# Performance work log

Hardware: AMD Instinct MI355X
Metric: run time of the kernel (lower is better)

The kernel has to match this reference:

```python
import jax, jax.numpy as jnp
import numpy as np

N = 50000        # nodes
E = 800000       # edges (before self loops)
NFEAT = 128
HEADS = 8
NHID = 16
SLOPE = 0.2      # PyG GATConv default negative_slope


def gat_conv(x, src, dst, W, a_src, a_dst, bias, heads, out_ch, concat):
    n = x.shape[0]
    h = (x @ W).reshape(n, heads, out_ch)                 # [N,H,C]
    al_s = jnp.sum(h * a_src, axis=-1)                    # [N,H]
    al_d = jnp.sum(h * a_dst, axis=-1)                    # [N,H]
    # add self loops (PyG GATConv default add_self_loops=True)
    loop = jnp.arange(n, dtype=src.dtype)
    s = jnp.concatenate([src, loop])
    d = jnp.concatenate([dst, loop])
    e = jax.nn.leaky_relu(al_s[s] + al_d[d], SLOPE)       # [E+N,H]
    # numerically stable softmax over incoming edges of each dst node
    emax = jax.lax.stop_gradient(jax.ops.segment_max(e, d, num_segments=n))
    ex = jnp.exp(e - emax[d])
    denom = jax.ops.segment_sum(ex, d, num_segments=n)
    alpha = ex / denom[d]                                 # [E+N,H]
    out = jax.ops.segment_sum(h[s] * alpha[:, :, None], d, num_segments=n)  # [N,H,C]
    out = out.reshape(n, heads * out_ch) if concat else out.mean(axis=1)
    return out + bias


def setup_inputs() -> dict:
    key = jax.random.key(0)
    ks = jax.random.split(key, 11)
    x = jax.random.normal(ks[0], (N, NFEAT), jnp.float32)
    src = jax.random.randint(ks[1], (E,), 0, N, dtype=jnp.int32)
    dst = jax.random.randint(ks[2], (E,), 0, N, dtype=jnp.int32)
    dst = jnp.where(src == dst, (dst + 1) % N, dst)  # no pre-existing self loops
    edge_index = jnp.stack([src, dst])
    sc = 0.1
    W1 = jax.random.normal(ks[3], (NFEAT, HEADS * NHID), jnp.float32) * sc
    a_src1 = jax.random.normal(ks[4], (HEADS, NHID), jnp.float32) * sc
    a_dst1 = jax.random.normal(ks[5], (HEADS, NHID), jnp.float32) * sc
    b1 = jnp.zeros((HEADS * NHID,), jnp.float32)
    W2 = jax.random.normal(ks[6], (HEADS * NHID, NHID), jnp.float32) * sc
    a_src2 = jax.random.normal(ks[7], (1, NHID), jnp.float32) * sc
    a_dst2 = jax.random.normal(ks[8], (1, NHID), jnp.float32) * sc
    b2 = jnp.zeros((NHID,), jnp.float32)
    return {"x": x, "edge_index": edge_index, "W1": W1, "a_src1": a_src1,
            "a_dst1": a_dst1, "b1": b1, "W2": W2, "a_src2": a_src2,
            "a_dst2": a_dst2, "b2": b2}


def reference(x, edge_index, W1, a_src1, a_dst1, b1, W2, a_src2, a_dst2, b2):
    src, dst = edge_index[0], edge_index[1]
    # layer 1: GATConv(nfeat -> nhid, heads=8, concat) + relu (dropout off in eval)
    h = jax.nn.relu(gat_conv(x, src, dst, W1, a_src1, a_dst1, b1, HEADS, NHID, True))
    # layer 2: GATConv(heads*nhid -> nhid, heads=1, concat=False) + relu
    out = jax.nn.relu(gat_conv(h, src, dst, W2, a_src2, a_dst2, b2, 1, NHID, False))
    return out
```

## Files before the change

kernel.cpp:

```cpp
#include <hip/hip_runtime.h>

#define NFEAT 128
#define HEADS 8
#define NHID 16
#define SLOPE 0.2f
#define BSH 8
#define CAPSH 13

typedef __fp16 f16x8 __attribute__((ext_vector_type(8)));
typedef __fp16 f16x2 __attribute__((ext_vector_type(2)));
typedef float  f4v   __attribute__((ext_vector_type(4)));

__device__ __forceinline__ unsigned pack2h(float a, float b) {
    union { f16x2 h; unsigned u; } r;
    r.h = __builtin_amdgcn_cvt_pkrtz(a, b);
    return r.u;
}
__device__ __forceinline__ f16x2 as_f16x2(unsigned u) {
    union { unsigned u; f16x2 h; } r; r.u = u; return r.h;
}
__device__ __forceinline__ f16x8 frag_from_f32(const float* p) {
    float4 q0 = *(const float4*)p;
    float4 q1 = *(const float4*)(p + 4);
    union { f16x8 v; f16x2 h[4]; } r;
    r.h[0] = __builtin_amdgcn_cvt_pkrtz(q0.x, q0.y);
    r.h[1] = __builtin_amdgcn_cvt_pkrtz(q0.z, q0.w);
    r.h[2] = __builtin_amdgcn_cvt_pkrtz(q1.x, q1.y);
    r.h[3] = __builtin_amdgcn_cvt_pkrtz(q1.z, q1.w);
    return r.v;
}


__global__ __launch_bounds__(256) void k_bscatter(const int* __restrict__ src,
                                                  const int* __restrict__ dst,
                                                  int E, int chunk,
                                                  int* __restrict__ bcount,
                                                  unsigned* __restrict__ pairs) {
    __shared__ int cnt[256], base[256];
    int t = threadIdx.x;
    int beg = blockIdx.x * chunk;
    int end = min(beg + chunk, E);
    if (beg >= end) return;
    cnt[t] = 0;
    __syncthreads();
    for (int i = beg + t; i < end; i += 256)
        atomicAdd(&cnt[dst[i] >> BSH], 1);
    __syncthreads();
    int c = cnt[t];
    base[t] = c ? (atomicAdd(&bcount[t], c) + (t << CAPSH)) : 0;
    __syncthreads();
    cnt[t] = 0;
    __syncthreads();
    for (int i = beg + t; i < end; i += 256) {
        int d = dst[i];
        int b = d >> BSH;
        int ofs = atomicAdd(&cnt[b], 1);
        pairs[base[b] + ofs] = (unsigned)src[i] | ((unsigned)(d & 255) << 16);
    }
}


__global__ __launch_bounds__(256) void k_scan_prep(const int* __restrict__ bcount,
                                                   int* __restrict__ cstart,
                                                   int* __restrict__ row_start,
                                                   int E, int n,
                                                   const float* __restrict__ W1,
                                                   const float* __restrict__ as1,
                                                   const float* __restrict__ ad1,
                                                   const float* __restrict__ W2,
                                                   unsigned* __restrict__ Wt1,
                                                   __fp16* __restrict__ Aat1,
                                                   unsigned* __restrict__ W2t) {
    if (blockIdx.x == 0) {
        __shared__ int sh[256];
        int t = threadIdx.x;
        int nb = (n + 255) >> BSH;
        int v = (t < nb) ? bcount[t] : 0;
        sh[t] = v;
        __syncthreads();
        for (int off = 1; off < 256; off <<= 1) {
            int u = (t >= off) ? sh[t - off] : 0;
            __syncthreads();
            sh[t] += u;
            __syncthreads();
        }
        cstart[t] = sh[t] - v;
        if (t == 0) row_start[n] = E + n;
        return;
    }
    int t = (blockIdx.x - 1) * 256 + threadIdx.x;
    if (t < 8192) {
        int c = t >> 6, m = t & 63;
        int k = 2 * m;
        Wt1[t] = pack2h(W1[k * 128 + c], W1[(k + 1) * 128 + c]);
    } else if (t < 10240) {
        int idx = t - 8192;
        int j = idx >> 7, k = idx & 127;
        float v = 0.f;
        if (j < 8)  { if ((k >> 4) == j)     v = as1[k]; }
        else        { if ((k >> 4) == j - 8) v = ad1[k]; }
        Aat1[idx] = (__fp16)v;
    } else if (t < 11264) {
        int idx = t - 10240;
        int c = idx >> 6, m = idx & 63;
        int k = 2 * m;
        W2t[idx] = pack2h(W2[k * 16 + c], W2[(k + 1) * 16 + c]);
    }
}


__global__ __launch_bounds__(256) void k_csr_gemm1(const unsigned* __restrict__ pairs,
                                                   const int* __restrict__ bcount,
                                                   const int* __restrict__ cstart,
                                                   int* __restrict__ row_start,
                                                   unsigned short* __restrict__ csr,
                                                   const float* __restrict__ xf,
                                                   const __fp16* __restrict__ Wt,
                                                   const __fp16* __restrict__ Aat,
                                                   unsigned* __restrict__ h1u,
                                                   float* __restrict__ als,
                                                   float* __restrict__ ald,
                                                   int n, int nbuck) {
    __shared__ unsigned smem[4][32 * 64];
    if ((int)blockIdx.x < nbuck) {
        int* deg = (int*)&smem[0][0];
        int* sc  = deg + 256;
        int b = blockIdx.x, t = threadIdx.x;
        int d0 = b << BSH;
        int nd = min(256, n - d0);
        deg[t] = (t < nd) ? 1 : 0;
        __syncthreads();
        int pbeg = b << CAPSH, pend = pbeg + bcount[b];
        for (int i = pbeg + t; i < pend; i += 256)
            atomicAdd(&deg[(pairs[i] >> 16) & 255], 1);
        __syncthreads();
        int v = deg[t];
        sc[t] = v;
        __syncthreads();
        for (int off = 1; off < 256; off <<= 1) {
            int u = (t >= off) ? sc[t - off] : 0;
            __syncthreads();
            sc[t] += u;
            __syncthreads();
        }
        int excl = sc[t] - v;
        int cbase = cstart[b] + d0;
        if (t < nd) row_start[d0 + t] = cbase + excl;
        __syncthreads();
        deg[t] = excl;
        __syncthreads();
        if (t < nd) {
            int pos = atomicAdd(&deg[t], 1);
            csr[cbase + pos] = (unsigned short)(d0 + t);
        }
        for (int i = pbeg + t; i < pend; i += 256) {
            unsigned p = pairs[i];
            int pos = atomicAdd(&deg[(p >> 16) & 255], 1);
            csr[cbase + pos] = (unsigned short)(p & 0xFFFFu);
        }
        return;
    }
    int bid = blockIdx.x - nbuck;
    int tid = threadIdx.x;
    int w = tid >> 6, l = tid & 63;
    int l15 = l & 15, lq = l >> 4;
    int wbase = bid * 128 + w * 32;
    f4v acc[2][8] = {};
    int r0 = min(wbase + l15, n - 1);
    int r1 = min(wbase + 16 + l15, n - 1);
#pragma unroll
    for (int kb = 0; kb < 4; ++kb) {
        int ko = kb * 32 + lq * 8;
        f16x8 a0 = frag_from_f32(&xf[(size_t)r0 * 128 + ko]);
        f16x8 a1 = frag_from_f32(&xf[(size_t)r1 * 128 + ko]);
#pragma unroll
        for (int cg = 0; cg < 8; ++cg) {
            f16x8 b = *(const f16x8*)&Wt[(size_t)(cg * 16 + l15) * 128 + ko];
            acc[0][cg] = __builtin_amdgcn_mfma_f32_16x16x32_f16(a0, b, acc[0][cg], 0, 0, 0);
            acc[1][cg] = __builtin_amdgcn_mfma_f32_16x16x32_f16(a1, b, acc[1][cg], 0, 0, 0);
        }
    }
    unsigned* myl = smem[w];
#pragma unroll
    for (int T = 0; T < 2; ++T) {
#pragma unroll
        for (int cg = 0; cg < 8; ++cg) {
#pragma unroll
            for (int j = 0; j < 4; ++j) {
                float v = acc[T][cg][j];
                float vo = __shfl_xor(v, 1);
                if ((l15 & 1) == 0) {
                    int nd = T * 16 + lq * 4 + j;
                    int wd = cg * 8 + (l15 >> 1);
                    int widx = nd * 64 + (((wd >> 2) ^ (nd & 15)) << 2) + (wd & 3);
                    myl[widx] = pack2h(v, vo);
                }
            }
        }
    }
    __syncthreads();
#pragma unroll
    for (int it = 0; it < 8; ++it) {
        int nd = it * 4 + lq;
        int node = wbase + nd;
        uint4 vv = *(const uint4*)&myl[nd * 64 + ((l15 ^ (nd & 15)) << 2)];
        if (node < n) *(uint4*)&h1u[(size_t)node * 64 + l15 * 4] = vv;
    }
#pragma unroll
    for (int T = 0; T < 2; ++T) {
        f4v acca = {};
#pragma unroll
        for (int kb = 0; kb < 4; ++kb) {
            int nd = T * 16 + l15;
            f16x8 ah = *(const f16x8*)&myl[nd * 64 + (((kb * 4 + lq) ^ (nd & 15)) << 2)];
            f16x8 bb = *(const f16x8*)&Aat[l15 * 128 + kb * 32 + lq * 8];
            acca = __builtin_amdgcn_mfma_f32_16x16x32_f16(ah, bb, acca, 0, 0, 0);
        }
#pragma unroll
        for (int j = 0; j < 4; ++j) {
            int node = wbase + T * 16 + lq * 4 + j;
            if (node < n) {
                if (l15 < 8) als[(size_t)node * 8 + l15] = acca[j];
                else         ald[(size_t)node * 8 + (l15 - 8)] = acca[j];
            }
        }
    }
}


__global__ __launch_bounds__(256) void k_agg1(const unsigned* __restrict__ hu,
                                              const float* __restrict__ als,
                                              const float* __restrict__ ald,
                                              const float* __restrict__ bias,
                                              const int* __restrict__ row_start,
                                              const unsigned short* __restrict__ csr,
                                              unsigned* __restrict__ out1u, int n) {
    int t = threadIdx.x;
    int l = t & 63;
    int lc = l & 15, eg = l >> 4;
    int nn = blockIdx.x * 4 + (t >> 6);
    if (nn >= n) return;
    int beg = row_start[nn], end = row_start[nn + 1];
    int len = end - beg;
    int g0 = beg + ((len * eg) >> 2);
    int g1 = beg + ((len * (eg + 1)) >> 2);
    int hd = lc >> 1;
    float aldv = ald[(size_t)nn * 8 + hd];
    float a[8] = {0.f, 0.f, 0.f, 0.f, 0.f, 0.f, 0.f, 0.f};
    float dn = 0.f;
    f16x2 one2; one2[0] = (__fp16)1.f; one2[1] = (__fp16)1.f;
    int i = g0;
    for (; i + 4 <= g1; i += 4) {
        int s0 = csr[i], s1 = csr[i + 1], s2 = csr[i + 2], s3 = csr[i + 3];
        float e0 = als[(size_t)s0 * 8 + hd];
        float e1 = als[(size_t)s1 * 8 + hd];
        float e2 = als[(size_t)s2 * 8 + hd];
        float e3 = als[(size_t)s3 * 8 + hd];
        uint4 v0 = *(const uint4*)&hu[(size_t)s0 * 64 + lc * 4];
        uint4 v1 = *(const uint4*)&hu[(size_t)s1 * 64 + lc * 4];
        uint4 v2 = *(const uint4*)&hu[(size_t)s2 * 64 + lc * 4];
        uint4 v3 = *(const uint4*)&hu[(size_t)s3 * 64 + lc * 4];
        e0 += aldv; e0 = (e0 < 0.f) ? SLOPE * e0 : e0;
        e1 += aldv; e1 = (e1 < 0.f) ? SLOPE * e1 : e1;
        e2 += aldv; e2 = (e2 < 0.f) ? SLOPE * e2 : e2;
        e3 += aldv; e3 = (e3 < 0.f) ? SLOPE * e3 : e3;
        f16x2 xa = __builtin_amdgcn_cvt_pkrtz(__expf(e0), __expf(e1));
        f16x2 xb = __builtin_amdgcn_cvt_pkrtz(__expf(e2), __expf(e3));
        dn = __builtin_amdgcn_fdot2(xa, one2, dn, false);
        dn = __builtin_amdgcn_fdot2(xb, one2, dn, false);
        unsigned V0[4] = {v0.x, v0.y, v0.z, v0.w};
        unsigned V1[4] = {v1.x, v1.y, v1.z, v1.w};
        unsigned V2[4] = {v2.x, v2.y, v2.z, v2.w};
        unsigned V3[4] = {v3.x, v3.y, v3.z, v3.w};
#pragma unroll
        for (int j = 0; j < 4; ++j) {
            unsigned lo01 = __builtin_amdgcn_perm(V1[j], V0[j], 0x05040100u);
            unsigned hi01 = __builtin_amdgcn_perm(V1[j], V0[j], 0x07060302u);
            unsigned lo23 = __builtin_amdgcn_perm(V3[j], V2[j], 0x05040100u);
            unsigned hi23 = __builtin_amdgcn_perm(V3[j], V2[j], 0x07060302u);
            a[2 * j]     = __builtin_amdgcn_fdot2(xa, as_f16x2(lo01), a[2 * j], false);
            a[2 * j + 1] = __builtin_amdgcn_fdot2(xa, as_f16x2(hi01), a[2 * j + 1], false);
            a[2 * j]     = __builtin_amdgcn_fdot2(xb, as_f16x2(lo23), a[2 * j], false);
            a[2 * j + 1] = __builtin_amdgcn_fdot2(xb, as_f16x2(hi23), a[2 * j + 1], false);
        }
    }
    for (; i + 2 <= g1; i += 2) {
        int s0 = csr[i];
        int s1 = csr[i + 1];
        float e0 = als[(size_t)s0 * 8 + hd];
        float e1 = als[(size_t)s1 * 8 + hd];
        uint4 v0 = *(const uint4*)&hu[(size_t)s0 * 64 + lc * 4];
        uint4 v1 = *(const uint4*)&hu[(size_t)s1 * 64 + lc * 4];
        e0 += aldv; e0 = (e0 < 0.f) ? SLOPE * e0 : e0;
        e1 += aldv; e1 = (e1 < 0.f) ? SLOPE * e1 : e1;
        f16x2 xx = __builtin_amdgcn_cvt_pkrtz(__expf(e0), __expf(e1));
        dn = __builtin_amdgcn_fdot2(xx, one2, dn, false);
        unsigned V0[4] = {v0.x, v0.y, v0.z, v0.w};
        unsigned V1[4] = {v1.x, v1.y, v1.z, v1.w};
#pragma unroll
        for (int j = 0; j < 4; ++j) {
            unsigned lo = __builtin_amdgcn_perm(V1[j], V0[j], 0x05040100u);
            unsigned hi = __builtin_amdgcn_perm(V1[j], V0[j], 0x07060302u);
            a[2 * j]     = __builtin_amdgcn_fdot2(xx, as_f16x2(lo), a[2 * j], false);
            a[2 * j + 1] = __builtin_amdgcn_fdot2(xx, as_f16x2(hi), a[2 * j + 1], false);
        }
    }
    if (i < g1) {
        int s0 = csr[i];
        float e0 = als[(size_t)s0 * 8 + hd] + aldv;
        uint4 v0 = *(const uint4*)&hu[(size_t)s0 * 64 + lc * 4];
        e0 = (e0 < 0.f) ? SLOPE * e0 : e0;
        float x0 = __expf(e0);
        dn += x0;
        unsigned V0[4] = {v0.x, v0.y, v0.z, v0.w};
#pragma unroll
        for (int j = 0; j < 4; ++j) {
            f16x2 p = as_f16x2(V0[j]);
            a[2 * j]     = fmaf(x0, (float)p[0], a[2 * j]);
            a[2 * j + 1] = fmaf(x0, (float)p[1], a[2 * j + 1]);
        }
    }
#pragma unroll
    for (int j = 0; j < 8; ++j) {
        a[j] += __shfl_xor(a[j], 16);
        a[j] += __shfl_xor(a[j], 32);
    }
    dn += __shfl_xor(dn, 16);
    dn += __shfl_xor(dn, 32);
    if (eg == 0) {
        float inv = 1.f / dn;
        float4 b0 = *(const float4*)&bias[lc * 8];
        float4 b1 = *(const float4*)&bias[lc * 8 + 4];
        uint4 o;
        o.x = pack2h(fmaxf(a[0] * inv + b0.x, 0.f), fmaxf(a[1] * inv + b0.y, 0.f));
        o.y = pack2h(fmaxf(a[2] * inv + b0.z, 0.f), fmaxf(a[3] * inv + b0.w, 0.f));
        o.z = pack2h(fmaxf(a[4] * inv + b1.x, 0.f), fmaxf(a[5] * inv + b1.y, 0.f));
        o.w = pack2h(fmaxf(a[6] * inv + b1.z, 0.f), fmaxf(a[7] * inv + b1.w, 0.f));
        *(uint4*)&out1u[(size_t)nn * 64 + lc * 4] = o;
    }
}


__global__ __launch_bounds__(256) void k_gemm2m(const __fp16* __restrict__ o1,
                                                const __fp16* __restrict__ W2t,
                                                const float* __restrict__ as2,
                                                const float* __restrict__ ad2,
                                                __fp16* __restrict__ h2,
                                                float* __restrict__ als,
                                                float* __restrict__ ald, int n) {
    int tid = threadIdx.x;
    int w = tid >> 6, l = tid & 63;
    int l15 = l & 15, lq = l >> 4;
    int wbase = blockIdx.x * 128 + w * 32;
    f4v acc[2] = {};
    int r0 = min(wbase + l15, n - 1);
    int r1 = min(wbase + 16 + l15, n - 1);
#pragma unroll
    for (int kb = 0; kb < 4; ++kb) {
        int ko = kb * 32 + lq * 8;
        f16x8 a0 = *(const f16x8*)&o1[(size_t)r0 * 128 + ko];
        f16x8 a1 = *(const f16x8*)&o1[(size_t)r1 * 128 + ko];
        f16x8 b  = *(const f16x8*)&W2t[(size_t)l15 * 128 + ko];
        acc[0] = __builtin_amdgcn_mfma_f32_16x16x32_f16(a0, b, acc[0], 0, 0, 0);
        acc[1] = __builtin_amdgcn_mfma_f32_16x16x32_f16(a1, b, acc[1], 0, 0, 0);
    }
    float asv = as2[l15], adv = ad2[l15];
#pragma unroll
    for (int T = 0; T < 2; ++T) {
#pragma unroll
        for (int j = 0; j < 4; ++j) {
            int node = wbase + T * 16 + lq * 4 + j;
            float hv = acc[T][j];
            float ps = hv * asv, pd = hv * adv;
            ps += __shfl_xor(ps, 1); ps += __shfl_xor(ps, 2);
            ps += __shfl_xor(ps, 4); ps += __shfl_xor(ps, 8);
            pd += __shfl_xor(pd, 1); pd += __shfl_xor(pd, 2);
            pd += __shfl_xor(pd, 4); pd += __shfl_xor(pd, 8);
            if (node < n) {
                h2[(size_t)node * 16 + l15] = (__fp16)hv;
                if (l15 == 0) { als[node] = ps; ald[node] = pd; }
            }
        }
    }
}


__global__ __launch_bounds__(256) void k_agg2(const __fp16* __restrict__ h,
                                              const float* __restrict__ als,
                                              const float* __restrict__ ald,
                                              const float* __restrict__ bias,
                                              const int* __restrict__ row_start,
                                              const unsigned short* __restrict__ csr,
                                              float* __restrict__ out, int n) {
    int t = threadIdx.x;
    int l = t & 63;
    int lc = l & 15, eg = l >> 4;
    int nn = blockIdx.x * 4 + (t >> 6);
    if (nn >= n) return;
    int beg = row_start[nn], end = row_start[nn + 1];
    int len = end - beg;
    int g0 = beg + ((len * eg) >> 2);
    int g1 = beg + ((len * (eg + 1)) >> 2);
    float aldv = ald[nn];
    float ac0 = 0.f, ac1 = 0.f, ac2 = 0.f, ac3 = 0.f;
    float dn0 = 0.f, dn1 = 0.f, dn2 = 0.f, dn3 = 0.f;
    int i = g0;
    for (; i + 4 <= g1; i += 4) {
        int s0 = csr[i], s1 = csr[i + 1], s2 = csr[i + 2], s3 = csr[i + 3];
        float e0 = als[s0], e1 = als[s1], e2 = als[s2], e3 = als[s3];
        float v0 = (float)h[(size_t)s0 * 16 + lc];
        float v1 = (float)h[(size_t)s1 * 16 + lc];
        float v2 = (float)h[(size_t)s2 * 16 + lc];
        float v3 = (float)h[(size_t)s3 * 16 + lc];
        e0 += aldv; e0 = (e0 < 0.f) ? SLOPE * e0 : e0;
        e1 += aldv; e1 = (e1 < 0.f) ? SLOPE * e1 : e1;
        e2 += aldv; e2 = (e2 < 0.f) ? SLOPE * e2 : e2;
        e3 += aldv; e3 = (e3 < 0.f) ? SLOPE * e3 : e3;
        float x0 = __expf(e0), x1 = __expf(e1), x2 = __expf(e2), x3 = __expf(e3);
        dn0 += x0; dn1 += x1; dn2 += x2; dn3 += x3;
        ac0 = fmaf(x0, v0, ac0);
        ac1 = fmaf(x1, v1, ac1);
        ac2 = fmaf(x2, v2, ac2);
        ac3 = fmaf(x3, v3, ac3);
    }
    for (; i < g1; ++i) {
        int s0 = csr[i];
        float e0 = als[s0] + aldv;
        e0 = (e0 < 0.f) ? SLOPE * e0 : e0;
        float x0 = __expf(e0);
        dn0 += x0;
        ac0 = fmaf(x0, (float)h[(size_t)s0 * 16 + lc], ac0);
    }
    float ac = (ac0 + ac1) + (ac2 + ac3);
    float dn = (dn0 + dn1) + (dn2 + dn3);
    ac += __shfl_xor(ac, 16); ac += __shfl_xor(ac, 32);
    dn += __shfl_xor(dn, 16); dn += __shfl_xor(dn, 32);
    if (eg == 0) out[(size_t)nn * 16 + lc] = fmaxf(ac / dn + bias[lc], 0.f);
}


extern "C" void kernel_launch(void* const* d_in, const int* in_sizes, int n_in,
                              void* d_out, int out_size, void* d_ws, size_t ws_size,
                              hipStream_t stream) {
    const float* x   = (const float*)d_in[0];
    const int*   ei  = (const int*)d_in[1];
    const float* W1  = (const float*)d_in[2];
    const float* as1 = (const float*)d_in[3];
    const float* ad1 = (const float*)d_in[4];
    const float* b1  = (const float*)d_in[5];
    const float* W2  = (const float*)d_in[6];
    const float* as2 = (const float*)d_in[7];
    const float* ad2 = (const float*)d_in[8];
    const float* b2  = (const float*)d_in[9];

    int N = in_sizes[0] / NFEAT;
    int E = in_sizes[1] / 2;
    const int* srcp = ei;
    const int* dstp = ei + E;
    int NBUCK = (N + 255) >> BSH;
    int NBg = (N + 127) / 128;

    char* ws = (char*)d_ws;
    size_t off = 0;
    auto take = [&](size_t bytes) -> char* {
        char* p = ws + off;
        off = (off + bytes + 255) & ~(size_t)255;
        return p;
    };
    int*            row_start = (int*)take((size_t)(N + 1) * 4);
    int*            bcount    = (int*)take(256 * 4);
    int*            cstart    = (int*)take(256 * 4);
    unsigned*       pairs     = (unsigned*)take((size_t)256 << (CAPSH + 2));
    unsigned short* csr       = (unsigned short*)take((size_t)(E + N) * 2);
    unsigned*       Wt1       = (unsigned*)take((size_t)128 * 64 * 4);
    __fp16*         Aat1      = (__fp16*)take((size_t)16 * 128 * 2);
    unsigned*       W2t       = (unsigned*)take((size_t)16 * 64 * 4);
    unsigned*       h1u       = (unsigned*)take((size_t)N * 64 * 4);
    float*          als1      = (float*)take((size_t)N * 8 * 4);
    float*          ald1      = (float*)take((size_t)N * 8 * 4);
    unsigned*       out1u     = (unsigned*)take((size_t)N * 64 * 4);
    __fp16*         h2        = (__fp16*)take((size_t)N * 16 * 2);
    float*          als2      = (float*)take((size_t)N * 4);
    float*          ald2      = (float*)take((size_t)N * 4);

    hipMemsetAsync(bcount, 0, 256 * 4, stream);
    int chunk = (E + 127) / 128;
    k_bscatter<<<128, 256, 0, stream>>>(srcp, dstp, E, chunk, bcount, pairs);
    k_scan_prep<<<45, 256, 0, stream>>>(bcount, cstart, row_start, E, N,
                                        W1, as1, ad1, W2, Wt1, Aat1, W2t);
    k_csr_gemm1<<<NBUCK + NBg, 256, 0, stream>>>(pairs, bcount, cstart, row_start, csr,
                                                 x, (const __fp16*)Wt1, Aat1,
                                                 h1u, als1, ald1, N, NBUCK);
    k_agg1<<<(N + 3) / 4, 256, 0, stream>>>(h1u, als1, ald1, b1, row_start, csr, out1u, N);
    k_gemm2m<<<NBg, 256, 0, stream>>>((const __fp16*)out1u, (const __fp16*)W2t,
                                      as2, ad2, h2, als2, ald2, N);
    k_agg2<<<(N + 3) / 4, 256, 0, stream>>>(h2, als2, ald2, b2, row_start, csr, (float*)d_out, N);
}
```

Baseline: 121.9 us.

## Fuse layer-2 projection into layer-1 aggregation and widen edge scatter grid

The layer-2 linear projection and attention-logit computation move into the epilogue of the layer-1 aggregation kernel. Each wave stages its aggregated fp16 row in shared memory and computes the 16 outputs with packed fp16 dot products. This removes the out1 intermediate round-trip through global memory and one kernel launch, at the cost of a longer epilogue and extra shuffles in the aggregation kernel. Separately, the edge bucket-scatter kernel is launched with twice as many blocks over smaller chunks.

```diff
diff --git a/kernel.cpp b/kernel.cpp
--- a/kernel.cpp
+++ b/kernel.cpp
@@ -234,11 +234,18 @@
                                               const float* __restrict__ bias,
                                               const int* __restrict__ row_start,
                                               const unsigned short* __restrict__ csr,
-                                              unsigned* __restrict__ out1u, int n) {
+                                              const unsigned* __restrict__ W2t,
+                                              const float* __restrict__ as2,
+                                              const float* __restrict__ ad2,
+                                              __fp16* __restrict__ h2,
+                                              float* __restrict__ als2,
+                                              float* __restrict__ ald2, int n) {
+    __shared__ unsigned lrow[4][64];
     int t = threadIdx.x;
+    int w = t >> 6;
     int l = t & 63;
     int lc = l & 15, eg = l >> 4;
-    int nn = blockIdx.x * 4 + (t >> 6);
+    int nn = blockIdx.x * 4 + w;
     if (nn >= n) return;
     int beg = row_start[nn], end = row_start[nn + 1];
     int len = end - beg;
@@ -327,8 +334,8 @@
     }
     dn += __shfl_xor(dn, 16);
     dn += __shfl_xor(dn, 32);
+    float inv = 1.f / dn;
     if (eg == 0) {
-        float inv = 1.f / dn;
         float4 b0 = *(const float4*)&bias[lc * 8];
         float4 b1 = *(const float4*)&bias[lc * 8 + 4];
         uint4 o;
@@ -336,52 +343,30 @@
         o.y = pack2h(fmaxf(a[2] * inv + b0.z, 0.f), fmaxf(a[3] * inv + b0.w, 0.f));
         o.z = pack2h(fmaxf(a[4] * inv + b1.x, 0.f), fmaxf(a[5] * inv + b1.y, 0.f));
         o.w = pack2h(fmaxf(a[6] * inv + b1.z, 0.f), fmaxf(a[7] * inv + b1.w, 0.f));
-        *(uint4*)&out1u[(size_t)nn * 64 + lc * 4] = o;
-    }
-}
-
-
-__global__ __launch_bounds__(256) void k_gemm2m(const __fp16* __restrict__ o1,
-                                                const __fp16* __restrict__ W2t,
-                                                const float* __restrict__ as2,
-                                                const float* __restrict__ ad2,
-                                                __fp16* __restrict__ h2,
-                                                float* __restrict__ als,
-                                                float* __restrict__ ald, int n) {
-    int tid = threadIdx.x;
-    int w = tid >> 6, l = tid & 63;
-    int l15 = l & 15, lq = l >> 4;
-    int wbase = blockIdx.x * 128 + w * 32;
-    f4v acc[2] = {};
-    int r0 = min(wbase + l15, n - 1);
-    int r1 = min(wbase + 16 + l15, n - 1);
-#pragma unroll
-    for (int kb = 0; kb < 4; ++kb) {
-        int ko = kb * 32 + lq * 8;
-        f16x8 a0 = *(const f16x8*)&o1[(size_t)r0 * 128 + ko];
-        f16x8 a1 = *(const f16x8*)&o1[(size_t)r1 * 128 + ko];
-        f16x8 b  = *(const f16x8*)&W2t[(size_t)l15 * 128 + ko];
-        acc[0] = __builtin_amdgcn_mfma_f32_16x16x32_f16(a0, b, acc[0], 0, 0, 0);
-        acc[1] = __builtin_amdgcn_mfma_f32_16x16x32_f16(a1, b, acc[1], 0, 0, 0);
-    }
-    float asv = as2[l15], adv = ad2[l15];
-#pragma unroll
-    for (int T = 0; T < 2; ++T) {
-#pragma unroll
-        for (int j = 0; j < 4; ++j) {
-            int node = wbase + T * 16 + lq * 4 + j;
-            float hv = acc[T][j];
-            float ps = hv * asv, pd = hv * adv;
-            ps += __shfl_xor(ps, 1); ps += __shfl_xor(ps, 2);
-            ps += __shfl_xor(ps, 4); ps += __shfl_xor(ps, 8);
-            pd += __shfl_xor(pd, 1); pd += __shfl_xor(pd, 2);
-            pd += __shfl_xor(pd, 4); pd += __shfl_xor(pd, 8);
-            if (node < n) {
-                h2[(size_t)node * 16 + l15] = (__fp16)hv;
-                if (l15 == 0) { als[node] = ps; ald[node] = pd; }
-            }
-        }
-    }
+        *(uint4*)&lrow[w][lc * 4] = o;
+    }
+    const uint4* rp = (const uint4*)&lrow[w][eg * 16];
+    const uint4* wp = (const uint4*)&W2t[lc * 64 + eg * 16];
+    float hp = 0.f;
+#pragma unroll
+    for (int q = 0; q < 4; ++q) {
+        uint4 rv = rp[q];
+        uint4 wv = wp[q];
+        hp = __builtin_amdgcn_fdot2(as_f16x2(rv.x), as_f16x2(wv.x), hp, false);
+        hp = __builtin_amdgcn_fdot2(as_f16x2(rv.y), as_f16x2(wv.y), hp, false);
+        hp = __builtin_amdgcn_fdot2(as_f16x2(rv.z), as_f16x2(wv.z), hp, false);
+        hp = __builtin_amdgcn_fdot2(as_f16x2(rv.w), as_f16x2(wv.w), hp, false);
+    }
+    hp += __shfl_xor(hp, 16);
+    hp += __shfl_xor(hp, 32);
+    float ps = hp * as2[lc];
+    float pd = hp * ad2[lc];
+    ps += __shfl_xor(ps, 1); ps += __shfl_xor(ps, 2);
+    ps += __shfl_xor(ps, 4); ps += __shfl_xor(ps, 8);
+    pd += __shfl_xor(pd, 1); pd += __shfl_xor(pd, 2);
+    pd += __shfl_xor(pd, 4); pd += __shfl_xor(pd, 8);
+    if (eg == 0) h2[(size_t)nn * 16 + lc] = (__fp16)hp;
+    if (l == 0) { als2[nn] = ps; ald2[nn] = pd; }
 }
 
 
@@ -478,21 +463,19 @@
     unsigned*       h1u       = (unsigned*)take((size_t)N * 64 * 4);
     float*          als1      = (float*)take((size_t)N * 8 * 4);
     float*          ald1      = (float*)take((size_t)N * 8 * 4);
-    unsigned*       out1u     = (unsigned*)take((size_t)N * 64 * 4);
     __fp16*         h2        = (__fp16*)take((size_t)N * 16 * 2);
     float*          als2      = (float*)take((size_t)N * 4);
     float*          ald2      = (float*)take((size_t)N * 4);
 
     hipMemsetAsync(bcount, 0, 256 * 4, stream);
-    int chunk = (E + 127) / 128;
-    k_bscatter<<<128, 256, 0, stream>>>(srcp, dstp, E, chunk, bcount, pairs);
+    int chunk = (E + 255) / 256;
+    k_bscatter<<<256, 256, 0, stream>>>(srcp, dstp, E, chunk, bcount, pairs);
     k_scan_prep<<<45, 256, 0, stream>>>(bcount, cstart, row_start, E, N,
                                         W1, as1, ad1, W2, Wt1, Aat1, W2t);
     k_csr_gemm1<<<NBUCK + NBg, 256, 0, stream>>>(pairs, bcount, cstart, row_start, csr,
                                                  x, (const __fp16*)Wt1, Aat1,
                                                  h1u, als1, ald1, N, NBUCK);
-    k_agg1<<<(N + 3) / 4, 256, 0, stream>>>(h1u, als1, ald1, b1, row_start, csr, out1u, N);
-    k_gemm2m<<<NBg, 256, 0, stream>>>((const __fp16*)out1u, (const __fp16*)W2t,
-                                      as2, ad2, h2, als2, ald2, N);
+    k_agg1<<<(N + 3) / 4, 256, 0, stream>>>(h1u, als1, ald1, b1, row_start, csr,
+                                            W2t, as2, ad2, h2, als2, ald2, N);
     k_agg2<<<(N + 3) / 4, 256, 0, stream>>>(h2, als2, ald2, b2, row_start, csr, (float*)d_out, N);
 }
```

New measurement: 120.5 us. About the same (-1.1%).

## Split layer-1 aggregation across two head-group blocks per node and widen scatter grid

Applied to the files above, without the earlier changes.

The layer-1 aggregation kernel now splits each node's 8 heads into two halves, each handled by a different block (blockIdx parity), so each wave processes two nodes with 8 channel lanes by 4 edge-splits instead of one node with 16 lanes. This doubles the number of blocks and halves the per-lane gather width per node, aiming for more parallelism and better latency hiding. The cost is that CSR indices and attention scores are read twice per node, once per head group. The bucket-scatter kernel launch is also doubled to 256 blocks with smaller chunks.

```diff
diff --git a/kernel.cpp b/kernel.cpp
--- a/kernel.cpp
+++ b/kernel.cpp
@@ -236,16 +236,21 @@
                                               const unsigned short* __restrict__ csr,
                                               unsigned* __restrict__ out1u, int n) {
     int t = threadIdx.x;
+    int w = t >> 6;
     int l = t & 63;
-    int lc = l & 15, eg = l >> 4;
-    int nn = blockIdx.x * 4 + (t >> 6);
+    int lc = l & 7;
+    int es = (l >> 3) & 3;
+    int ns = l >> 5;
+    int g = blockIdx.x & 1;
+    int nn = (blockIdx.x >> 1) * 8 + w * 2 + ns;
     if (nn >= n) return;
+    const unsigned* hg = hu + g * 32;
+    int hd = g * 4 + (lc >> 1);
+    float aldv = ald[(size_t)nn * 8 + hd];
     int beg = row_start[nn], end = row_start[nn + 1];
     int len = end - beg;
-    int g0 = beg + ((len * eg) >> 2);
-    int g1 = beg + ((len * (eg + 1)) >> 2);
-    int hd = lc >> 1;
-    float aldv = ald[(size_t)nn * 8 + hd];
+    int g0 = beg + ((len * es) >> 2);
+    int g1 = beg + ((len * (es + 1)) >> 2);
     float a[8] = {0.f, 0.f, 0.f, 0.f, 0.f, 0.f, 0.f, 0.f};
     float dn = 0.f;
     f16x2 one2; one2[0] = (__fp16)1.f; one2[1] = (__fp16)1.f;
@@ -256,10 +261,10 @@
         float e1 = als[(size_t)s1 * 8 + hd];
         float e2 = als[(size_t)s2 * 8 + hd];
         float e3 = als[(size_t)s3 * 8 + hd];
-        uint4 v0 = *(const uint4*)&hu[(size_t)s0 * 64 + lc * 4];
-        uint4 v1 = *(const uint4*)&hu[(size_t)s1 * 64 + lc * 4];
-        uint4 v2 = *(const uint4*)&hu[(size_t)s2 * 64 + lc * 4];
-        uint4 v3 = *(const uint4*)&hu[(size_t)s3 * 64 + lc * 4];
+        uint4 v0 = *(const uint4*)&hg[(size_t)s0 * 64 + lc * 4];
+        uint4 v1 = *(const uint4*)&hg[(size_t)s1 * 64 + lc * 4];
+        uint4 v2 = *(const uint4*)&hg[(size_t)s2 * 64 + lc * 4];
+        uint4 v3 = *(const uint4*)&hg[(size_t)s3 * 64 + lc * 4];
         e0 += aldv; e0 = (e0 < 0.f) ? SLOPE * e0 : e0;
         e1 += aldv; e1 = (e1 < 0.f) ? SLOPE * e1 : e1;
         e2 += aldv; e2 = (e2 < 0.f) ? SLOPE * e2 : e2;
@@ -289,8 +294,8 @@
         int s1 = csr[i + 1];
         float e0 = als[(size_t)s0 * 8 + hd];
         float e1 = als[(size_t)s1 * 8 + hd];
-        uint4 v0 = *(const uint4*)&hu[(size_t)s0 * 64 + lc * 4];
-        uint4 v1 = *(const uint4*)&hu[(size_t)s1 * 64 + lc * 4];
+        uint4 v0 = *(const uint4*)&hg[(size_t)s0 * 64 + lc * 4];
+        uint4 v1 = *(const uint4*)&hg[(size_t)s1 * 64 + lc * 4];
         e0 += aldv; e0 = (e0 < 0.f) ? SLOPE * e0 : e0;
         e1 += aldv; e1 = (e1 < 0.f) ? SLOPE * e1 : e1;
         f16x2 xx = __builtin_amdgcn_cvt_pkrtz(__expf(e0), __expf(e1));
@@ -308,7 +313,7 @@
     if (i < g1) {
         int s0 = csr[i];
         float e0 = als[(size_t)s0 * 8 + hd] + aldv;
-        uint4 v0 = *(const uint4*)&hu[(size_t)s0 * 64 + lc * 4];
+        uint4 v0 = *(const uint4*)&hg[(size_t)s0 * 64 + lc * 4];
         e0 = (e0 < 0.f) ? SLOPE * e0 : e0;
         float x0 = __expf(e0);
         dn += x0;
@@ -322,21 +327,22 @@
     }
 #pragma unroll
     for (int j = 0; j < 8; ++j) {
+        a[j] += __shfl_xor(a[j], 8);
         a[j] += __shfl_xor(a[j], 16);
-        a[j] += __shfl_xor(a[j], 32);
-    }
+    }
+    dn += __shfl_xor(dn, 8);
     dn += __shfl_xor(dn, 16);
-    dn += __shfl_xor(dn, 32);
-    if (eg == 0) {
+    if (es == 0) {
         float inv = 1.f / dn;
-        float4 b0 = *(const float4*)&bias[lc * 8];
-        float4 b1 = *(const float4*)&bias[lc * 8 + 4];
+        int ch = g * 64 + lc * 8;
+        float4 b0 = *(const float4*)&bias[ch];
+        float4 b1 = *(const float4*)&bias[ch + 4];
         uint4 o;
         o.x = pack2h(fmaxf(a[0] * inv + b0.x, 0.f), fmaxf(a[1] * inv + b0.y, 0.f));
         o.y = pack2h(fmaxf(a[2] * inv + b0.z, 0.f), fmaxf(a[3] * inv + b0.w, 0.f));
         o.z = pack2h(fmaxf(a[4] * inv + b1.x, 0.f), fmaxf(a[5] * inv + b1.y, 0.f));
         o.w = pack2h(fmaxf(a[6] * inv + b1.z, 0.f), fmaxf(a[7] * inv + b1.w, 0.f));
-        *(uint4*)&out1u[(size_t)nn * 64 + lc * 4] = o;
+        *(uint4*)&out1u[(size_t)nn * 64 + g * 32 + lc * 4] = o;
     }
 }
 
@@ -484,14 +490,15 @@
     float*          ald2      = (float*)take((size_t)N * 4);
 
     hipMemsetAsync(bcount, 0, 256 * 4, stream);
-    int chunk = (E + 127) / 128;
-    k_bscatter<<<128, 256, 0, stream>>>(srcp, dstp, E, chunk, bcount, pairs);
+    int chunk = (E + 255) / 256;
+    k_bscatter<<<256, 256, 0, stream>>>(srcp, dstp, E, chunk, bcount, pairs);
     k_scan_prep<<<45, 256, 0, stream>>>(bcount, cstart, row_start, E, N,
                                         W1, as1, ad1, W2, Wt1, Aat1, W2t);
     k_csr_gemm1<<<NBUCK + NBg, 256, 0, stream>>>(pairs, bcount, cstart, row_start, csr,
                                                  x, (const __fp16*)Wt1, Aat1,
                                                  h1u, als1, ald1, N, NBUCK);
-    k_agg1<<<(N + 3) / 4, 256, 0, stream>>>(h1u, als1, ald1, b1, row_start, csr, out1u, N);
+    int nb1 = ((N + 7) / 8) * 2;
+    k_agg1<<<nb1, 256, 0, stream>>>(h1u, als1, ald1, b1, row_start, csr, out1u, N);
     k_gemm2m<<<NBg, 256, 0, stream>>>((const __fp16*)out1u, (const __fp16*)W2t,
                                       as2, ad2, h2, als2, ald2, N);
     k_agg2<<<(N + 3) / 4, 256, 0, stream>>>(h2, als2, ald2, b2, row_start, csr, (float*)d_out, N);
```

After: 112.7 us (median of 2 runs). -7.5%, faster.
